# Kernel tuning notes

Hardware: AMD Instinct MI355X
Metric: run time of the kernel (lower is better)

Reference implementation:

```python
import jax, jax.numpy as jnp
import numpy as np

WS = 16  # window_size


def setup_inputs() -> dict:
    key = jax.random.key(0)
    ks = jax.random.split(key, 5)
    B, C, H, W = 4, 192, 256, 256
    x = jax.random.normal(ks[0], (B, C, H, W), dtype=jnp.float32)
    w_qkv = jax.random.normal(ks[1], (3 * C, C), dtype=jnp.float32) * 0.02
    b_qkv = jnp.zeros((3 * C,), dtype=jnp.float32)
    w_pe = jax.random.normal(ks[2], (C, 1, 3, 3), dtype=jnp.float32) * 0.02  # depthwise: OIHW with I=1, groups=C
    b_pe = jnp.zeros((C,), dtype=jnp.float32)
    w_out = jax.random.normal(ks[3], (C, C), dtype=jnp.float32) * 0.02
    b_out = jnp.zeros((C,), dtype=jnp.float32)
    return {"x": x, "w_qkv": w_qkv, "b_qkv": b_qkv, "w_pe": w_pe,
            "b_pe": b_pe, "w_out": w_out, "b_out": b_out}


def reference(x, w_qkv, b_qkv, w_pe, b_pe, w_out, b_out):
    ws = WS
    B, C, H, W = x.shape
    # window_partition: faithful to torch .view on contiguous NCHW tensor
    xw = x.reshape(B, H // ws, ws, W // ws, ws, C)
    xw = jnp.transpose(xw, (0, 1, 3, 2, 4, 5)).reshape(-1, ws * ws, C)  # (N, ws^2, C)
    # QKV projection (torch Linear: x @ W.T + b)
    qkv = xw @ w_qkv.T + b_qkv
    q, k, v = jnp.split(qkv, 3, axis=-1)
    N = q.shape[0]
    # LePE: pure reshape (as in original), then depthwise 3x3 conv
    vimg = v.reshape(N, C, ws, ws)
    lepe = jax.lax.conv_general_dilated(
        vimg, w_pe, window_strides=(1, 1), padding="SAME",
        feature_group_count=C,
        dimension_numbers=("NCHW", "OIHW", "NCHW"))
    lepe = lepe + b_pe[None, :, None, None]
    lepe = lepe.reshape(N, ws * ws, C)
    # scaled dot-product attention per window (no heads; scale = 1/sqrt(C))
    scale = 1.0 / jnp.sqrt(jnp.asarray(C, x.dtype))
    scores = jnp.einsum("nqc,nkc->nqk", q, k) * scale
    attn = jax.nn.softmax(scores, axis=-1)
    o = jnp.einsum("nqk,nkc->nqc", attn, v) + lepe
    # output projection
    o = o @ w_out.T + b_out
    # reverse_window_partition: faithful reshape/permute/reshape
    o = o.reshape(B, H // ws, W // ws, ws, ws, C)
    o = jnp.transpose(o, (0, 1, 3, 2, 4, 5)).reshape(B, -1, H, W)
    return o
```

## Files before the change

### kernel.cpp

```cpp
#include <hip/hip_runtime.h>

typedef unsigned short u16;
typedef short bf16x8 __attribute__((ext_vector_type(8)));
typedef float f32x4 __attribute__((ext_vector_type(4)));

__device__ __forceinline__ u16 f2b(float f) {
  union { float f; unsigned u; } v; v.f = f;
  unsigned r = v.u + 0x7FFFu + ((v.u >> 16) & 1u);
  return (u16)(r >> 16);
}
__device__ __forceinline__ float b2f(u16 h) {
  union { unsigned u; float f; } v; v.u = ((unsigned)h) << 16;
  return v.f;
}

template <int R, int K, int T>
__device__ __forceinline__ void stage_f32(const float* __restrict__ src, int rowStride,
                                          char* lds, int tid) {
  constexpr int CPR = K / 4;
  constexpr int CHUNKS = R * CPR;
  #pragma unroll
  for (int ci = tid; ci < CHUNKS; ci += T) {
    int r = ci / CPR, u = ci % CPR;
    float4 vv = *reinterpret_cast<const float4*>(src + (size_t)r * rowStride + u * 4);
    ushort4 h;
    h.x = f2b(vv.x); h.y = f2b(vv.y); h.z = f2b(vv.z); h.w = f2b(vv.w);
    int bc = (u * 8) ^ ((r & 7) << 4);
    *reinterpret_cast<ushort4*>(lds + r * (2 * K) + bc) = h;
  }
}

template <int R, int K, int T>
__device__ __forceinline__ void stage_b16(const u16* __restrict__ src, int rowStride,
                                          char* lds, int tid) {
  constexpr int CPR = K / 8;
  constexpr int CHUNKS = R * CPR;
  #pragma unroll
  for (int ci = tid; ci < CHUNKS; ci += T) {
    int r = ci / CPR, u = ci % CPR;
    int4 vv = *reinterpret_cast<const int4*>(src + (size_t)r * rowStride + u * 8);
    int bc = (u * 16) ^ ((r & 7) << 4);
    *reinterpret_cast<int4*>(lds + r * (2 * K) + bc) = vv;
  }
}

template <int KC, int FM, int FN, int FNT>
__device__ __forceinline__ void mma_chunk(const char* ldsA, const char* ldsB, int lane,
                                          int wm0, int wn0, int jo, f32x4 (&acc)[FM][FNT]) {
  constexpr int LD = 2 * KC;
  #pragma unroll
  for (int ks = 0; ks < KC / 32; ++ks) {
    bf16x8 a[FM], b[FN];
    int kb = ks * 64 + ((lane >> 4) << 4);
    #pragma unroll
    for (int i = 0; i < FM; ++i) {
      int row = wm0 + i * 16 + (lane & 15);
      a[i] = *reinterpret_cast<const bf16x8*>(ldsA + row * LD + (kb ^ ((row & 7) << 4)));
    }
    #pragma unroll
    for (int j = 0; j < FN; ++j) {
      int row = wn0 + j * 16 + (lane & 15);
      b[j] = *reinterpret_cast<const bf16x8*>(ldsB + row * LD + (kb ^ ((row & 7) << 4)));
    }
    #pragma unroll
    for (int i = 0; i < FM; ++i)
      #pragma unroll
      for (int j = 0; j < FN; ++j)
        acc[i][jo + j] =
            __builtin_amdgcn_mfma_f32_16x16x32_bf16(a[i], b[j], acc[i][jo + j], 0, 0, 0);
  }
}

__global__ __launch_bounds__(256) void k_qkv(const float* __restrict__ x,
                                             const float* __restrict__ wqkv,
                                             const float* __restrict__ bqkv,
                                             u16* __restrict__ q, u16* __restrict__ kk,
                                             u16* __restrict__ v) {
  __shared__ __align__(16) char ldsA[128 * 384];
  __shared__ __align__(16) char ldsB[64 * 384];
  int tid = threadIdx.x;
  stage_f32<128, 192, 256>(x + (size_t)blockIdx.x * (128 * 192), 192, ldsA, tid);
  int lane = tid & 63, wid = tid >> 6;
  int wm0 = wid * 32;
  int colL = lane & 15, rq = (lane >> 4) * 4;
  #pragma unroll 1
  for (int ch = 0; ch < 9; ++ch) {
    if (ch) __syncthreads();
    stage_f32<64, 192, 256>(wqkv + ch * (64 * 192), 192, ldsB, tid);
    __syncthreads();
    f32x4 acc[2][4];
    #pragma unroll
    for (int i = 0; i < 2; ++i)
      #pragma unroll
      for (int j = 0; j < 4; ++j)
        #pragma unroll
        for (int e = 0; e < 4; ++e) acc[i][j][e] = 0.f;
    mma_chunk<192, 2, 4, 4>(ldsA, ldsB, lane, wm0, 0, 0, acc);
    u16* dst;
    int pbase = ch * 64;
    if (ch < 3) dst = q;
    else if (ch < 6) { dst = kk; pbase -= 192; }
    else { dst = v; pbase -= 384; }
    #pragma unroll
    for (int j = 0; j < 4; ++j) {
      int pc = pbase + j * 16 + colL;
      float bias = bqkv[ch * 64 + j * 16 + colL];
      #pragma unroll
      for (int i = 0; i < 2; ++i)
        #pragma unroll
        for (int rr = 0; rr < 4; ++rr) {
          int m = blockIdx.x * 128 + wm0 + i * 16 + rq + rr;
          int b = m >> 16, i1 = (m >> 12) & 15, i2 = (m >> 8) & 15, i3 = (m >> 4) & 15,
              i4 = m & 15;
          int w = (((((b << 4) | i1) << 4) | i3) << 8) | (i2 << 4) | i4;
          dst[(size_t)w * 192 + pc] = f2b(acc[i][j][rr] + bias);
        }
    }
  }
}

__global__ __launch_bounds__(512) void k_fused(const u16* __restrict__ q,
                                               const u16* __restrict__ kk,
                                               const u16* __restrict__ v,
                                               u16* __restrict__ o) {
  __shared__ __align__(16) char lds[147456];
  char* ldsQ = lds;
  char* ldsK = lds + 98304;
  char* ldsP = lds;
  char* ldsV = lds + 131072;
  int tid = threadIdx.x, z = blockIdx.x;
  int lane = tid & 63, wid = tid >> 6;
  int wm0 = wid * 32;
  const u16* qb = q + (size_t)z * 49152;
  const u16* kb = kk + (size_t)z * 49152;
  const u16* vb = v + (size_t)z * 49152;
  u16* ob = o + (size_t)z * 49152;

  stage_b16<256, 192, 512>(qb, 192, ldsQ, tid);
  stage_b16<128, 192, 512>(kb, 192, ldsK, tid);
  int4 kreg[6];
  #pragma unroll
  for (int s = 0; s < 6; ++s) {
    int ci = tid + s * 512;
    int r = ci / 24, u = ci % 24;
    kreg[s] = *reinterpret_cast<const int4*>(kb + (size_t)(128 + r) * 192 + u * 8);
  }
  f32x4 acc[2][16];
  #pragma unroll
  for (int i = 0; i < 2; ++i)
    #pragma unroll
    for (int j = 0; j < 16; ++j)
      #pragma unroll
      for (int e = 0; e < 4; ++e) acc[i][j][e] = 0.f;
  __syncthreads();
  mma_chunk<192, 2, 8, 16>(ldsQ, ldsK, lane, wm0, 0, 0, acc);
  __syncthreads();
  #pragma unroll
  for (int s = 0; s < 6; ++s) {
    int ci = tid + s * 512;
    int r = ci / 24, u = ci % 24;
    *reinterpret_cast<int4*>(ldsK + r * 384 + ((u * 16) ^ ((r & 7) << 4))) = kreg[s];
  }
  __syncthreads();
  mma_chunk<192, 2, 8, 16>(ldsQ, ldsK, lane, wm0, 0, 8, acc);
  __syncthreads();

  int4 vreg[2];
  #pragma unroll
  for (int s = 0; s < 2; ++s) {
    int ci = tid + s * 512;
    int tt = ci >> 2, u = ci & 3;
    vreg[s] = *reinterpret_cast<const int4*>(vb + (size_t)tt * 192 + u * 8);
  }

  const float scale = 0.07216878364870323f;
  int colL = lane & 15, rq = (lane >> 4) * 4;
  #pragma unroll
  for (int i = 0; i < 2; ++i)
    #pragma unroll
    for (int rr = 0; rr < 4; ++rr) {
      float m = -1e30f;
      #pragma unroll
      for (int j = 0; j < 16; ++j) m = fmaxf(m, acc[i][j][rr]);
      #pragma unroll
      for (int off = 8; off; off >>= 1) m = fmaxf(m, __shfl_xor(m, off));
      float s = 0.f;
      #pragma unroll
      for (int j = 0; j < 16; ++j) {
        float e = __expf((acc[i][j][rr] - m) * scale);
        acc[i][j][rr] = e;
        s += e;
      }
      #pragma unroll
      for (int off = 8; off; off >>= 1) s += __shfl_xor(s, off);
      float iv = 1.0f / s;
      int row = wm0 + i * 16 + rq + rr;
      int swz = (row & 7) << 4;
      #pragma unroll
      for (int j = 0; j < 16; ++j) {
        int tc = j * 16 + colL;
        *reinterpret_cast<u16*>(ldsP + row * 512 + ((tc * 2) ^ swz)) =
            f2b(acc[i][j][rr] * iv);
      }
    }

  #pragma unroll 1
  for (int cc = 0; cc < 6; ++cc) {
    __syncthreads();
    #pragma unroll
    for (int s = 0; s < 2; ++s) {
      int ci = tid + s * 512;
      int tt = ci >> 2, u = ci & 3;
      unsigned w0 = (unsigned)vreg[s].x, w1 = (unsigned)vreg[s].y,
               w2 = (unsigned)vreg[s].z, w3 = (unsigned)vreg[s].w;
      int tb = tt * 2;
      char* base = ldsV + u * 8 * 512;
      *reinterpret_cast<u16*>(base + 0 * 512 + (tb ^ 0x00)) = (u16)(w0 & 0xFFFF);
      *reinterpret_cast<u16*>(base + 1 * 512 + (tb ^ 0x10)) = (u16)(w0 >> 16);
      *reinterpret_cast<u16*>(base + 2 * 512 + (tb ^ 0x20)) = (u16)(w1 & 0xFFFF);
      *reinterpret_cast<u16*>(base + 3 * 512 + (tb ^ 0x30)) = (u16)(w1 >> 16);
      *reinterpret_cast<u16*>(base + 4 * 512 + (tb ^ 0x40)) = (u16)(w2 & 0xFFFF);
      *reinterpret_cast<u16*>(base + 5 * 512 + (tb ^ 0x50)) = (u16)(w2 >> 16);
      *reinterpret_cast<u16*>(base + 6 * 512 + (tb ^ 0x60)) = (u16)(w3 & 0xFFFF);
      *reinterpret_cast<u16*>(base + 7 * 512 + (tb ^ 0x70)) = (u16)(w3 >> 16);
    }
    if (cc < 5) {
      #pragma unroll
      for (int s = 0; s < 2; ++s) {
        int ci = tid + s * 512;
        int tt = ci >> 2, u = ci & 3;
        vreg[s] =
            *reinterpret_cast<const int4*>(vb + (size_t)tt * 192 + (cc + 1) * 32 + u * 8);
      }
    }
    __syncthreads();
    f32x4 acc2[2][2];
    #pragma unroll
    for (int i = 0; i < 2; ++i)
      #pragma unroll
      for (int j = 0; j < 2; ++j)
        #pragma unroll
        for (int e = 0; e < 4; ++e) acc2[i][j][e] = 0.f;
    mma_chunk<256, 2, 2, 2>(ldsP, ldsV, lane, wm0, 0, 0, acc2);
    #pragma unroll
    for (int i = 0; i < 2; ++i)
      #pragma unroll
      for (int j = 0; j < 2; ++j)
        #pragma unroll
        for (int rr = 0; rr < 4; ++rr) {
          int row = wm0 + i * 16 + rq + rr;
          ob[row * 192 + cc * 32 + j * 16 + colL] = f2b(acc2[i][j][rr]);
        }
  }
}

__global__ __launch_bounds__(256) void k_lepe(const u16* __restrict__ v,
                                              u16* __restrict__ o,
                                              const float* __restrict__ wpe,
                                              const float* __restrict__ bpe) {
  __shared__ __align__(16) char lds[64 * 520];
  int tid = threadIdx.x;
  int g = blockIdx.x, z = blockIdx.y;
  const u16* vb = v + (size_t)z * 49152 + g * 16384;
  #pragma unroll
  for (int s = 0; s < 8; ++s) {
    int ci = tid + s * 256;
    int4 vv = *reinterpret_cast<const int4*>(vb + ci * 8);
    char* dst = lds + (ci >> 5) * 520 + (ci & 31) * 16;
    int2 lo, hi;
    lo.x = vv.x; lo.y = vv.y; hi.x = vv.z; hi.y = vv.w;
    *reinterpret_cast<int2*>(dst) = lo;
    *reinterpret_cast<int2*>(dst + 8) = hi;
  }
  __syncthreads();
  int p = tid & 63;
  int a = tid >> 6;
  int cp = g * 64 + p;
  float w[9];
  #pragma unroll
  for (int i = 0; i < 9; ++i) w[i] = wpe[cp * 9 + i];
  float bias = bpe[cp];
  const char* Lp = lds + p * 520;
  float R[6][16];
  #pragma unroll
  for (int rr = 0; rr < 6; ++rr) {
    int row = a * 4 - 1 + rr;
    if (row >= 0 && row < 16) {
      #pragma unroll
      for (int c = 0; c < 4; ++c) {
        uint2 d = *reinterpret_cast<const uint2*>(Lp + row * 32 + c * 8);
        R[rr][c * 4 + 0] = b2f((u16)(d.x & 0xFFFF));
        R[rr][c * 4 + 1] = b2f((u16)(d.x >> 16));
        R[rr][c * 4 + 2] = b2f((u16)(d.y & 0xFFFF));
        R[rr][c * 4 + 3] = b2f((u16)(d.y >> 16));
      }
    } else {
      #pragma unroll
      for (int xx = 0; xx < 16; ++xx) R[rr][xx] = 0.f;
    }
  }
  u16* ob = o + (size_t)z * 49152 + g * 16384 + p * 256 + a * 64;
  #pragma unroll
  for (int rr = 0; rr < 4; ++rr) {
    float accr[16];
    #pragma unroll
    for (int xx = 0; xx < 16; ++xx) {
      float s = bias;
      #pragma unroll
      for (int dy = 0; dy < 3; ++dy) {
        if (xx > 0) s += w[dy * 3 + 0] * R[rr + dy][xx - 1];
        s += w[dy * 3 + 1] * R[rr + dy][xx];
        if (xx < 15) s += w[dy * 3 + 2] * R[rr + dy][xx + 1];
      }
      accr[xx] = s;
    }
    #pragma unroll
    for (int hh = 0; hh < 2; ++hh) {
      int4 ov = *reinterpret_cast<int4*>(ob + rr * 16 + hh * 8);
      unsigned* owp = reinterpret_cast<unsigned*>(&ov);
      #pragma unroll
      for (int c = 0; c < 4; ++c) {
        unsigned word = owp[c];
        float lo = b2f((u16)(word & 0xFFFF)) + accr[hh * 8 + c * 2];
        float hi2 = b2f((u16)(word >> 16)) + accr[hh * 8 + c * 2 + 1];
        owp[c] = (unsigned)f2b(lo) | ((unsigned)f2b(hi2) << 16);
      }
      *reinterpret_cast<int4*>(ob + rr * 16 + hh * 8) = ov;
    }
  }
}

__global__ __launch_bounds__(256) void k_outproj(const u16* __restrict__ o,
                                                 const float* __restrict__ wout,
                                                 const float* __restrict__ bout,
                                                 float* __restrict__ out) {
  __shared__ __align__(16) char ldsA[128 * 384];
  __shared__ __align__(16) char ldsB[64 * 384];
  int tid = threadIdx.x;
  stage_b16<128, 192, 256>(o + (size_t)blockIdx.x * (128 * 192), 192, ldsA, tid);
  int lane = tid & 63, wid = tid >> 6;
  int wm0 = wid * 32;
  int colL = lane & 15, rq = (lane >> 4) * 4;
  #pragma unroll 1
  for (int ch = 0; ch < 3; ++ch) {
    if (ch) __syncthreads();
    stage_f32<64, 192, 256>(wout + ch * (64 * 192), 192, ldsB, tid);
    __syncthreads();
    f32x4 acc[2][4];
    #pragma unroll
    for (int i = 0; i < 2; ++i)
      #pragma unroll
      for (int j = 0; j < 4; ++j)
        #pragma unroll
        for (int e = 0; e < 4; ++e) acc[i][j][e] = 0.f;
    mma_chunk<192, 2, 4, 4>(ldsA, ldsB, lane, wm0, 0, 0, acc);
    #pragma unroll
    for (int j = 0; j < 4; ++j) {
      int p = ch * 64 + j * 16 + colL;
      float bias = bout[p];
      #pragma unroll
      for (int i = 0; i < 2; ++i)
        #pragma unroll
        for (int rr = 0; rr < 4; ++rr) {
          int w = blockIdx.x * 128 + wm0 + i * 16 + rq + rr;
          int n = w >> 8, t = w & 255;
          int b = n >> 8, i1 = (n >> 4) & 15, i3 = n & 15, i2 = t >> 4, i4 = t & 15;
          int jj = (((((((b << 4) | i1) << 4) | i2) << 4) | i3) << 4) | i4;
          out[(size_t)jj * 192 + p] = acc[i][j][rr] + bias;
        }
    }
  }
}

extern "C" void kernel_launch(void* const* d_in, const int* in_sizes, int n_in,
                              void* d_out, int out_size, void* d_ws, size_t ws_size,
                              hipStream_t stream) {
  const float* x = (const float*)d_in[0];
  const float* w_qkv = (const float*)d_in[1];
  const float* b_qkv = (const float*)d_in[2];
  const float* w_pe = (const float*)d_in[3];
  const float* b_pe = (const float*)d_in[4];
  const float* w_out = (const float*)d_in[5];
  const float* b_out = (const float*)d_in[6];
  float* out = (float*)d_out;
  char* ws = (char*)d_ws;

  u16* q = (u16*)(ws + 0);
  u16* k = (u16*)(ws + 100663296);
  u16* v = (u16*)(ws + 201326592);
  u16* o = (u16*)(ws + 301989888);

  k_qkv<<<dim3(2048), 256, 0, stream>>>(x, w_qkv, b_qkv, q, k, v);
  k_fused<<<dim3(1024), 512, 0, stream>>>(q, k, v, o);
  k_lepe<<<dim3(3, 1024), 256, 0, stream>>>(v, o, w_pe, b_pe);
  k_outproj<<<dim3(2048), 256, 0, stream>>>(o, w_out, b_out, out);
}
```

Before: 862.2 us.

## Pre-convert projection weights to bf16 and register-prefetch next weight chunk

Adds a small kernel that converts w_qkv and w_out to bf16 once per call into scratch space. The QKV and output-projection GEMMs then load bf16 weight chunks directly, prefetching the next chunk into registers while the current one is in LDS. Scattered output row offsets are computed once before the chunk loop. This halves weight load bytes and removes per-chunk fp32-to-bf16 conversion, at the cost of two extra launches and scratch buffers. One buffer sits inside the output tensor and is later overwritten, the other reuses the q region.

After: 843.0 us. -2.2%, faster.

```diff
diff --git a/kernel.cpp b/kernel.cpp
--- a/kernel.cpp
+++ b/kernel.cpp
@@ -71,8 +71,19 @@
   }
 }
 
+__global__ __launch_bounds__(256) void k_f2b(const float* __restrict__ src,
+                                             u16* __restrict__ dst, int n) {
+  int i = (blockIdx.x * 256 + threadIdx.x) * 4;
+  if (i < n) {
+    float4 vv = *reinterpret_cast<const float4*>(src + i);
+    ushort4 h;
+    h.x = f2b(vv.x); h.y = f2b(vv.y); h.z = f2b(vv.z); h.w = f2b(vv.w);
+    *reinterpret_cast<ushort4*>(dst + i) = h;
+  }
+}
+
 __global__ __launch_bounds__(256) void k_qkv(const float* __restrict__ x,
-                                             const float* __restrict__ wqkv,
+                                             const u16* __restrict__ wb,
                                              const float* __restrict__ bqkv,
                                              u16* __restrict__ q, u16* __restrict__ kk,
                                              u16* __restrict__ v) {
@@ -83,10 +94,42 @@
   int lane = tid & 63, wid = tid >> 6;
   int wm0 = wid * 32;
   int colL = lane & 15, rq = (lane >> 4) * 4;
+  int wrow[8];
+  #pragma unroll
+  for (int i = 0; i < 2; ++i)
+    #pragma unroll
+    for (int rr = 0; rr < 4; ++rr) {
+      int m = blockIdx.x * 128 + wm0 + i * 16 + rq + rr;
+      int b = m >> 16, i1 = (m >> 12) & 15, i2 = (m >> 8) & 15, i3 = (m >> 4) & 15,
+          i4 = m & 15;
+      int w = (((((b << 4) | i1) << 4) | i3) << 8) | (i2 << 4) | i4;
+      wrow[i * 4 + rr] = w * 192;
+    }
+  int4 breg[6];
+  #pragma unroll
+  for (int s = 0; s < 6; ++s) {
+    int ci = tid + s * 256;
+    int r = ci / 24, u = ci % 24;
+    breg[s] = *reinterpret_cast<const int4*>(wb + r * 192 + u * 8);
+  }
   #pragma unroll 1
   for (int ch = 0; ch < 9; ++ch) {
     if (ch) __syncthreads();
-    stage_f32<64, 192, 256>(wqkv + ch * (64 * 192), 192, ldsB, tid);
+    #pragma unroll
+    for (int s = 0; s < 6; ++s) {
+      int ci = tid + s * 256;
+      int r = ci / 24, u = ci % 24;
+      *reinterpret_cast<int4*>(ldsB + r * 384 + ((u * 16) ^ ((r & 7) << 4))) = breg[s];
+    }
+    if (ch < 8) {
+      #pragma unroll
+      for (int s = 0; s < 6; ++s) {
+        int ci = tid + s * 256;
+        int r = ci / 24, u = ci % 24;
+        breg[s] =
+            *reinterpret_cast<const int4*>(wb + (ch + 1) * 12288 + r * 192 + u * 8);
+      }
+    }
     __syncthreads();
     f32x4 acc[2][4];
     #pragma unroll
@@ -108,13 +151,8 @@
       #pragma unroll
       for (int i = 0; i < 2; ++i)
         #pragma unroll
-        for (int rr = 0; rr < 4; ++rr) {
-          int m = blockIdx.x * 128 + wm0 + i * 16 + rq + rr;
-          int b = m >> 16, i1 = (m >> 12) & 15, i2 = (m >> 8) & 15, i3 = (m >> 4) & 15,
-              i4 = m & 15;
-          int w = (((((b << 4) | i1) << 4) | i3) << 8) | (i2 << 4) | i4;
-          dst[(size_t)w * 192 + pc] = f2b(acc[i][j][rr] + bias);
-        }
+        for (int rr = 0; rr < 4; ++rr)
+          dst[(size_t)(wrow[i * 4 + rr] + pc)] = f2b(acc[i][j][rr] + bias);
     }
   }
 }
@@ -331,7 +369,7 @@
 }
 
 __global__ __launch_bounds__(256) void k_outproj(const u16* __restrict__ o,
-                                                 const float* __restrict__ wout,
+                                                 const u16* __restrict__ wbo,
                                                  const float* __restrict__ bout,
                                                  float* __restrict__ out) {
   __shared__ __align__(16) char ldsA[128 * 384];
@@ -341,10 +379,42 @@
   int lane = tid & 63, wid = tid >> 6;
   int wm0 = wid * 32;
   int colL = lane & 15, rq = (lane >> 4) * 4;
+  int jjoff[8];
+  #pragma unroll
+  for (int i = 0; i < 2; ++i)
+    #pragma unroll
+    for (int rr = 0; rr < 4; ++rr) {
+      int w = blockIdx.x * 128 + wm0 + i * 16 + rq + rr;
+      int n = w >> 8, t = w & 255;
+      int b = n >> 8, i1 = (n >> 4) & 15, i3 = n & 15, i2 = t >> 4, i4 = t & 15;
+      int jj = (((((((b << 4) | i1) << 4) | i2) << 4) | i3) << 4) | i4;
+      jjoff[i * 4 + rr] = jj * 192;
+    }
+  int4 breg[6];
+  #pragma unroll
+  for (int s = 0; s < 6; ++s) {
+    int ci = tid + s * 256;
+    int r = ci / 24, u = ci % 24;
+    breg[s] = *reinterpret_cast<const int4*>(wbo + r * 192 + u * 8);
+  }
   #pragma unroll 1
   for (int ch = 0; ch < 3; ++ch) {
     if (ch) __syncthreads();
-    stage_f32<64, 192, 256>(wout + ch * (64 * 192), 192, ldsB, tid);
+    #pragma unroll
+    for (int s = 0; s < 6; ++s) {
+      int ci = tid + s * 256;
+      int r = ci / 24, u = ci % 24;
+      *reinterpret_cast<int4*>(ldsB + r * 384 + ((u * 16) ^ ((r & 7) << 4))) = breg[s];
+    }
+    if (ch < 2) {
+      #pragma unroll
+      for (int s = 0; s < 6; ++s) {
+        int ci = tid + s * 256;
+        int r = ci / 24, u = ci % 24;
+        breg[s] =
+            *reinterpret_cast<const int4*>(wbo + (ch + 1) * 12288 + r * 192 + u * 8);
+      }
+    }
     __syncthreads();
     f32x4 acc[2][4];
     #pragma unroll
@@ -361,13 +431,8 @@
       #pragma unroll
       for (int i = 0; i < 2; ++i)
         #pragma unroll
-        for (int rr = 0; rr < 4; ++rr) {
-          int w = blockIdx.x * 128 + wm0 + i * 16 + rq + rr;
-          int n = w >> 8, t = w & 255;
-          int b = n >> 8, i1 = (n >> 4) & 15, i3 = n & 15, i2 = t >> 4, i4 = t & 15;
-          int jj = (((((((b << 4) | i1) << 4) | i2) << 4) | i3) << 4) | i4;
-          out[(size_t)jj * 192 + p] = acc[i][j][rr] + bias;
-        }
+        for (int rr = 0; rr < 4; ++rr)
+          out[(size_t)(jjoff[i * 4 + rr] + p)] = acc[i][j][rr] + bias;
     }
   }
 }
@@ -389,9 +454,13 @@
   u16* k = (u16*)(ws + 100663296);
   u16* v = (u16*)(ws + 201326592);
   u16* o = (u16*)(ws + 301989888);
-
-  k_qkv<<<dim3(2048), 256, 0, stream>>>(x, w_qkv, b_qkv, q, k, v);
+  u16* wb = (u16*)((char*)d_out + 190000000);
+  u16* wbo = (u16*)(ws + 0);
+
+  k_f2b<<<dim3(108), 256, 0, stream>>>(w_qkv, wb, 110592);
+  k_qkv<<<dim3(2048), 256, 0, stream>>>(x, wb, b_qkv, q, k, v);
   k_fused<<<dim3(1024), 512, 0, stream>>>(q, k, v, o);
+  k_f2b<<<dim3(36), 256, 0, stream>>>(w_out, wbo, 36864);
   k_lepe<<<dim3(3, 1024), 256, 0, stream>>>(v, o, w_pe, b_pe);
-  k_outproj<<<dim3(2048), 256, 0, stream>>>(o, w_out, b_out, out);
-}
+  k_outproj<<<dim3(2048), 256, 0, stream>>>(o, wbo, b_out, out);
+}
```
